# Optimization experiments

Measured on AMD Instinct MI355X. Metric: run time of the kernel, lower is better.

## Reference

```python
import jax, jax.numpy as jnp
import numpy as np

BN_EPS = 1e-5


def conv(x, w, b=None, stride=1, pad=1):
    out = jax.lax.conv_general_dilated(
        x, w, (stride, stride), [(pad, pad), (pad, pad)],
        dimension_numbers=("NCHW", "OIHW", "NCHW"))
    if b is not None:
        out = out + b[None, :, None, None]
    return out


def bn_relu(x):
    # BatchNorm2d(affine=False) in training mode: per-channel batch stats
    mean = jnp.mean(x, axis=(0, 2, 3), keepdims=True)
    var = jnp.var(x, axis=(0, 2, 3), keepdims=True)
    return jax.nn.relu((x - mean) * jax.lax.rsqrt(var + BN_EPS))


def deform_conv(x, offset, w, b, stride, pad=1):
    # torchvision DeformConv2d semantics, 3x3 kernel, dilation=1
    B, C, H, W = x.shape
    O = w.shape[0]
    K = 9
    Ho, Wo = offset.shape[2], offset.shape[3]
    off = offset.reshape(B, K, 2, Ho, Wo)  # (dy, dx) per kernel tap
    ky, kx = jnp.meshgrid(jnp.arange(3), jnp.arange(3), indexing="ij")
    ky = ky.reshape(K).astype(x.dtype)
    kx = kx.reshape(K).astype(x.dtype)
    oy = (jnp.arange(Ho) * stride - pad).astype(x.dtype)
    ox = (jnp.arange(Wo) * stride - pad).astype(x.dtype)
    # sampling coords [B,K,Ho,Wo]
    ys = oy[None, None, :, None] + ky[None, :, None, None] + off[:, :, 0]
    xs = ox[None, None, None, :] + kx[None, :, None, None] + off[:, :, 1]
    y0 = jnp.floor(ys)
    x0 = jnp.floor(xs)
    wy1 = ys - y0
    wx1 = xs - x0
    imf = x.reshape(B, C, H * W)

    def gather(iy, ix):
        valid = (iy >= 0) & (iy <= H - 1) & (ix >= 0) & (ix <= W - 1)
        iyc = jnp.clip(iy, 0, H - 1).astype(jnp.int32)
        ixc = jnp.clip(ix, 0, W - 1).astype(jnp.int32)
        lin = iyc * W + ixc  # [B,K,Ho,Wo]
        g = jax.vmap(lambda im, li: im[:, li])(imf, lin)  # [B,C,K,Ho,Wo]
        return g * valid[:, None].astype(x.dtype)

    sampled = (gather(y0, x0) * ((1 - wy1) * (1 - wx1))[:, None]
               + gather(y0, x0 + 1) * ((1 - wy1) * wx1)[:, None]
               + gather(y0 + 1, x0) * (wy1 * (1 - wx1))[:, None]
               + gather(y0 + 1, x0 + 1) * (wy1 * wx1)[:, None])
    out = jnp.einsum("ock,bckhw->bohw", w.reshape(O, C, K), sampled)
    return out + b[None, :, None, None]


def avgpool4(x):
    B, C, H, W = x.shape
    return x.reshape(B, C, H // 4, 4, W // 4, 4).mean(axis=(3, 5))


def setup_inputs() -> dict:
    key = jax.random.key(0)
    ks = jax.random.split(key, 20)
    n = jax.random.normal
    s = 0.05
    return {
        "x": n(ks[0], (8, 3, 640, 640), jnp.float32),
        "w_off1": n(ks[1], (18, 3, 3, 3), jnp.float32) * s,
        "b_off1": jnp.zeros((18,), jnp.float32),
        "w_d1": n(ks[2], (64, 3, 3, 3), jnp.float32) * s,
        "b_d1": jnp.zeros((64,), jnp.float32),
        "w_skip": n(ks[3], (64, 3, 1, 1), jnp.float32) * s,
        "b_skip": jnp.zeros((64,), jnp.float32),
        "w_bl1": n(ks[4], (64, 64, 3, 3), jnp.float32) * s,
        "w_bl2": n(ks[5], (64, 64, 3, 3), jnp.float32) * s,
        "w_off2": n(ks[6], (18, 64, 3, 3), jnp.float32) * s,
        "b_off2": jnp.zeros((18,), jnp.float32),
        "w_d2": n(ks[7], (64, 64, 3, 3), jnp.float32) * s,
        "b_d2": jnp.zeros((64,), jnp.float32),
        "w_off3": n(ks[8], (18, 64, 3, 3), jnp.float32) * s,
        "b_off3": jnp.zeros((18,), jnp.float32),
        "w_d3": n(ks[9], (256, 64, 3, 3), jnp.float32) * s,
        "b_d3": jnp.zeros((256,), jnp.float32),
    }


def reference(x, w_off1, b_off1, w_d1, b_d1, w_skip, b_skip, w_bl1, w_bl2,
              w_off2, b_off2, w_d2, b_d2, w_off3, b_off3, w_d3, b_d3):
    offset1 = conv(x, w_off1, b_off1, stride=4)
    d1 = deform_conv(x, offset1, w_d1, b_d1, stride=4)
    skip = conv(avgpool4(x), w_skip, b_skip, stride=1, pad=0)
    f = bn_relu(conv(d1 + skip, w_bl1))
    feat_1_4 = bn_relu(conv(f, w_bl2))
    offset2 = conv(feat_1_4, w_off2, b_off2, stride=2)
    feat_1_8 = deform_conv(feat_1_4, offset2, w_d2, b_d2, stride=2)
    offset3 = conv(feat_1_8, w_off3, b_off3, stride=2)
    feat_1_16 = deform_conv(feat_1_8, offset3, w_d3, b_d3, stride=2)
    return (feat_1_4, feat_1_8, feat_1_16)
```

## Files before the change

### kernel.cpp

```cpp
#include <hip/hip_runtime.h>
#include <hip/hip_bf16.h>
#include <math.h>

#define TPB 256

typedef __attribute__((ext_vector_type(8))) short bf16x8_t;
typedef __attribute__((ext_vector_type(4))) float f32x4_t;
typedef __attribute__((ext_vector_type(4))) int i32x4_t;
typedef __attribute__((ext_vector_type(4))) unsigned short u16x4_t;

static __device__ __forceinline__ float bf16_to_f(unsigned short s) {
    union { unsigned u; float f; } cv;
    cv.u = ((unsigned)s) << 16;
    return cv.f;
}
static __device__ __forceinline__ short f_to_bf16(float v) {
    __hip_bfloat16 h = __float2bfloat16(v);
    return *(short*)&h;
}

__global__ void repack_frag_kernel(const float* __restrict__ w,
                                   short* __restrict__ wtf,
                                   int Oreal, int NFRAG)
{
    int idx = blockIdx.x * TPB + threadIdx.x;
    int total = 18 * NFRAG * 64 * 8;
    if (idx >= total) return;
    int j    = idx & 7;
    int lane = (idx >> 3) & 63;
    int t    = idx >> 9;
    int ocf  = t % NFRAG;
    int kc   = t / NFRAG;
    int oc   = ocf * 16 + (lane & 15);
    int tap  = kc >> 1;
    int ic   = (kc & 1) * 32 + (lane >> 4) * 8 + j;
    float v = 0.f;
    if (oc < Oreal)
        v = w[((size_t)(oc * 64 + ic)) * 9 + tap];
    wtf[idx] = f_to_bf16(v);
}

__global__ __launch_bounds__(256, 2) void conv3x3_mfma_kernel(
    const short* __restrict__ xh,
    const short* __restrict__ wt,
    short* __restrict__ outh,
    float* __restrict__ stats,
    const float* __restrict__ zp)
{
    __shared__ short tile[2816 * 8];
    __shared__ float sstat[128];
    const int H = 160, W = 160, HW = 25600;
    int blk = blockIdx.x;
    int b  = blk / 100;
    int r  = blk % 100;
    int y0 = (r / 10) * 16;
    int x0 = (r % 10) * 16;
    const int tid = threadIdx.x;
    const short* inb = xh + (size_t)b * HW * 64;

#pragma unroll
    for (int it = 0; it < 11; ++it) {
        int item = it * 256 + tid;
        int c8  = item & 7;
        int pix = item >> 3;
        int row = pix / 18;
        int col = pix - row * 18;
        int y = y0 + row - 1;
        int x = x0 + col - 1;
        bool ok = (pix < 324) & (y >= 0) & (y < H) & (x >= 0) & (x < W);
        const short* src = ok
            ? &inb[((size_t)y * W + x) * 64 + ((c8 ^ (col & 7)) << 3)]
            : (const short*)zp;
        *(bf16x8_t*)&tile[item * 8] = *(const bf16x8_t*)src;
    }
    if (tid < 128) sstat[tid] = 0.f;
    __syncthreads();

    const int wv  = tid >> 6;
    const int l   = tid & 63;
    const int l15 = l & 15;
    const int lg  = l >> 4;

    f32x4_t acc[4][4];
#pragma unroll
    for (int i = 0; i < 4; ++i)
#pragma unroll
        for (int j = 0; j < 4; ++j)
            acc[i][j] = (f32x4_t){0.f, 0.f, 0.f, 0.f};

    bf16x8_t bfp[2][4], afp[2][4];
#pragma unroll
    for (int nf = 0; nf < 4; ++nf)
        bfp[0][nf] = *(const bf16x8_t*)(wt + (((size_t)(0 * 4 + nf)) * 64 + l) * 8);
    {
        int colr = l15;
        int chunk = lg ^ (colr & 7);
#pragma unroll
        for (int mf = 0; mf < 4; ++mf)
            afp[0][mf] = *(const bf16x8_t*)&tile[((wv * 4 + mf) * 18 + colr) * 64 + chunk * 8];
    }
#pragma unroll
    for (int kc = 0; kc < 18; ++kc) {
        const int cur = kc & 1, nxt = cur ^ 1;
        if (kc + 1 < 18) {
            int kn = kc + 1;
#pragma unroll
            for (int nf = 0; nf < 4; ++nf)
                bfp[nxt][nf] = *(const bf16x8_t*)(wt + (((size_t)(kn * 4 + nf)) * 64 + l) * 8);
            int tap = kn >> 1;
            int dy = tap / 3, dx = tap % 3;
            int colr = l15 + dx;
            int chunk = (((kn & 1) << 2) + lg) ^ (colr & 7);
#pragma unroll
            for (int mf = 0; mf < 4; ++mf)
                afp[nxt][mf] = *(const bf16x8_t*)&tile[((wv * 4 + mf + dy) * 18 + colr) * 64 + chunk * 8];
        }
#pragma unroll
        for (int mf = 0; mf < 4; ++mf)
#pragma unroll
            for (int nf = 0; nf < 4; ++nf)
                acc[mf][nf] = __builtin_amdgcn_mfma_f32_16x16x32_bf16(
                    afp[cur][mf], bfp[cur][nf], acc[mf][nf], 0, 0, 0);
    }

    __syncthreads();
#pragma unroll
    for (int mf = 0; mf < 4; ++mf) {
        int py = wv * 4 + mf;
#pragma unroll
        for (int nf = 0; nf < 4; ++nf) {
            int oc = nf * 16 + l15;
#pragma unroll
            for (int k = 0; k < 4; ++k)
                tile[((py * 16) + lg * 4 + k) * 64 + oc] = f_to_bf16(acc[mf][nf][k]);
        }
    }
    __syncthreads();
    short* outb = outh + (size_t)b * HW * 64;
#pragma unroll
    for (int j = 0; j < 8; ++j) {
        int item = j * 256 + tid;
        int c8  = item & 7;
        int pix = item >> 3;
        int py  = pix >> 4, px = pix & 15;
        *(bf16x8_t*)&outb[((size_t)(y0 + py) * W + x0 + px) * 64 + c8 * 8] =
            *(bf16x8_t*)&tile[pix * 64 + c8 * 8];
    }

#pragma unroll
    for (int nf = 0; nf < 4; ++nf) {
        float s = 0.f, s2 = 0.f;
#pragma unroll
        for (int mf = 0; mf < 4; ++mf)
#pragma unroll
            for (int k = 0; k < 4; ++k) {
                float v = acc[mf][nf][k];
                s += v; s2 += v * v;
            }
        s  += __shfl_xor(s, 16, 64);  s  += __shfl_xor(s, 32, 64);
        s2 += __shfl_xor(s2, 16, 64); s2 += __shfl_xor(s2, 32, 64);
        if (lg == 0) {
            int oc = nf * 16 + l15;
            atomicAdd(&sstat[oc], s);
            atomicAdd(&sstat[64 + oc], s2);
        }
    }
    __syncthreads();
    float* st = stats + (size_t)(blockIdx.x & 7) * 128;
    if (tid < 128) atomicAdd(&st[tid], sstat[tid]);
}

__global__ void nchw_to_nhwc_bf16_kernel(const float* __restrict__ in,
                                         short* __restrict__ out, int HW)
{
    __shared__ short tile[64][66];
    int nchunks = HW >> 6;
    int b  = blockIdx.x / nchunks;
    int p0 = (blockIdx.x % nchunks) << 6;
    int tid = threadIdx.x;
#pragma unroll
    for (int rep = 0; rep < 16; ++rep) {
        int item = rep * 256 + tid;
        int c = item >> 6, p = item & 63;
        tile[p][c] = f_to_bf16(in[((size_t)b * 64 + c) * HW + p0 + p]);
    }
    __syncthreads();
#pragma unroll
    for (int rep = 0; rep < 16; ++rep) {
        int item = rep * 256 + tid;
        int p = item >> 6, c = item & 63;
        out[((size_t)b * HW + p0 + p) * 64 + c] = tile[p][c];
    }
}

__global__ void bn_apply_elem_kernel(const short* __restrict__ in,
                                     const float* __restrict__ stats,
                                     short* __restrict__ outh,
                                     float invN)
{
    __shared__ float sm[64], sr[64];
    int tid = threadIdx.x;
    if (tid < 64) {
        float s = 0.f, s2 = 0.f;
#pragma unroll
        for (int k = 0; k < 8; ++k) {
            s  += stats[k * 128 + tid];
            s2 += stats[k * 128 + 64 + tid];
        }
        float mean = s * invN;
        float var  = s2 * invN - mean * mean;
        sm[tid] = mean;
        sr[tid] = rsqrtf(var + 1e-5f);
    }
    __syncthreads();
    int item = blockIdx.x * TPB + tid;
    int c0 = (item & 7) * 8;
    bf16x8_t v = *(const bf16x8_t*)&in[(size_t)item * 8];
    bf16x8_t o;
#pragma unroll
    for (int j = 0; j < 8; ++j) {
        float f = (bf16_to_f((unsigned short)v[j]) - sm[c0 + j]) * sr[c0 + j];
        o[j] = f_to_bf16(f > 0.f ? f : 0.f);
    }
    *(bf16x8_t*)&outh[(size_t)item * 8] = o;
}

__global__ void bn_apply_dual_kernel(const short* __restrict__ in,
                                     const float* __restrict__ stats,
                                     float* __restrict__ out,
                                     short* __restrict__ outh,
                                     int HW, float invN)
{
    __shared__ float ftile[64][65];
    __shared__ float sm[64], sr[64];
    int nchunks = HW >> 6;
    int b  = blockIdx.x / nchunks;
    int p0 = (blockIdx.x % nchunks) << 6;
    int tid = threadIdx.x;
    if (tid < 64) {
        float s = 0.f, s2 = 0.f;
#pragma unroll
        for (int k = 0; k < 8; ++k) {
            s  += stats[k * 128 + tid];
            s2 += stats[k * 128 + 64 + tid];
        }
        float mean = s * invN;
        float var  = s2 * invN - mean * mean;
        sm[tid] = mean;
        sr[tid] = rsqrtf(var + 1e-5f);
    }
    __syncthreads();
#pragma unroll
    for (int it = 0; it < 2; ++it) {
        int item = it * 256 + tid;
        int p = item >> 3, c0 = (item & 7) * 8;
        size_t gi = ((size_t)(b * HW + p0 + p)) * 64 + c0;
        bf16x8_t v = *(const bf16x8_t*)&in[gi];
        bf16x8_t o;
#pragma unroll
        for (int j = 0; j < 8; ++j) {
            float f = (bf16_to_f((unsigned short)v[j]) - sm[c0 + j]) * sr[c0 + j];
            f = f > 0.f ? f : 0.f;
            ftile[p][c0 + j] = f;
            o[j] = f_to_bf16(f);
        }
        *(bf16x8_t*)&outh[gi] = o;
    }
    __syncthreads();
#pragma unroll
    for (int rep = 0; rep < 16; ++rep) {
        int item = rep * 256 + tid;
        int c = item >> 6, p = item & 63;
        out[((size_t)b * 64 + c) * HW + p0 + p] = ftile[p][c];
    }
}

__global__ void x_to_nhwc4_kernel(const float* __restrict__ in,
                                  float* __restrict__ out)
{
    int idx = blockIdx.x * TPB + threadIdx.x;
    const int HW = 640 * 640;
    if (idx >= 8 * HW) return;
    int b = idx / HW, p = idx % HW;
    f32x4_t v;
    v[0] = in[((size_t)b * 3 + 0) * HW + p];
    v[1] = in[((size_t)b * 3 + 1) * HW + p];
    v[2] = in[((size_t)b * 3 + 2) * HW + p];
    v[3] = 0.f;
    *(f32x4_t*)&out[(size_t)idx * 4] = v;
}

__global__ void offset1_kernel(const float* __restrict__ x4,
                               const float* __restrict__ w,
                               const float* __restrict__ bias,
                               float* __restrict__ out)
{
    const int H = 640, W = 640, HW = 25600;
    int idx = blockIdx.x * TPB + threadIdx.x;
    if (idx >= 8 * HW) return;
    int b = idx / HW, r = idx % HW;
    int ho = r / 160, wo = r % 160;

    float acc[18];
#pragma unroll
    for (int o = 0; o < 18; ++o) acc[o] = bias[o];

    const float* xb = x4 + (size_t)b * H * W * 4;
#pragma unroll
    for (int tap = 0; tap < 9; ++tap) {
        int iy = ho * 4 - 1 + tap / 3;
        int ix = wo * 4 - 1 + tap % 3;
        if (iy < 0 || iy >= H || ix < 0 || ix >= W) continue;
        f32x4_t s = *(const f32x4_t*)&xb[((size_t)iy * W + ix) * 4];
#pragma unroll
        for (int c = 0; c < 3; ++c)
#pragma unroll
            for (int o = 0; o < 18; ++o)
                acc[o] += s[c] * w[(o * 3 + c) * 9 + tap];
    }
#pragma unroll
    for (int o = 0; o < 18; ++o)
        out[((size_t)(b * 18 + o)) * HW + r] = acc[o];
}

__global__ __launch_bounds__(256, 1) void offconv_mfma_kernel(
    const short* __restrict__ xh,
    const short* __restrict__ wt,
    const float* __restrict__ bias,
    float* __restrict__ out,
    int H, int W, int Ho, int Wo)
{
    const int HW = Ho * Wo;
    const int tid = threadIdx.x;
    const int wv = tid >> 6, l = tid & 63;
    const int l15 = l & 15, lg = l >> 4;
    const int pix0 = blockIdx.x * 64 + wv * 16;
    const int b = pix0 / HW;
    const int r0 = pix0 - b * HW;

    int rp = r0 + l15;
    int ho = rp / Wo, wo = rp % Wo;
    const short* xb = xh + (size_t)b * H * W * 64;

    f32x4_t acc[2];
    acc[0] = (f32x4_t){0.f, 0.f, 0.f, 0.f};
    acc[1] = (f32x4_t){0.f, 0.f, 0.f, 0.f};

#pragma unroll 2
    for (int kc = 0; kc < 18; ++kc) {
        int tap = kc >> 1;
        int iy = ho * 2 - 1 + tap / 3;
        int ix = wo * 2 - 1 + tap % 3;
        bf16x8_t af = {};
        if (iy >= 0 && iy < H && ix >= 0 && ix < W)
            af = *(const bf16x8_t*)&xb[((size_t)iy * W + ix) * 64
                                       + (kc & 1) * 32 + lg * 8];
#pragma unroll
        for (int nf = 0; nf < 2; ++nf) {
            bf16x8_t bf = *(const bf16x8_t*)(wt + (((size_t)(kc * 2 + nf)) * 64 + l) * 8);
            acc[nf] = __builtin_amdgcn_mfma_f32_16x16x32_bf16(af, bf, acc[nf], 0, 0, 0);
        }
    }

#pragma unroll
    for (int nf = 0; nf < 2; ++nf) {
        int oc = nf * 16 + l15;
        if (oc < 18) {
            float bv = bias[oc];
            f32x4_t v = acc[nf];
            v[0] += bv; v[1] += bv; v[2] += bv; v[3] += bv;
            *(f32x4_t*)&out[((size_t)(b * 18 + oc)) * HW + r0 + lg * 4] = v;
        }
    }
}

__global__ __launch_bounds__(256, 1) void deform1_kernel(
    const float* __restrict__ x4,
    const float* __restrict__ off,
    const float* __restrict__ w,
    const float* __restrict__ bias,
    const float* __restrict__ pool,
    const float* __restrict__ wsk,
    const float* __restrict__ bsk,
    short* __restrict__ outh)
{
    const int H = 640, W = 640, Ho = 160, Wo = 160, HW = 25600;
    constexpr int P = 32;
    __shared__ float samp[P][28];
    __shared__ int   sidx[P * 9][4];
    __shared__ float swt[P * 9][4];
    const int tid = threadIdx.x;
    const int pix0 = blockIdx.x * P;
    const int b = pix0 / HW;
    const int r0 = pix0 - b * HW;

    for (int item = tid; item < P * 9; item += TPB) {
        int p = item / 9, tap = item % 9;
        int r = r0 + p, ho = r / Wo, wo = r % Wo;
        float dy = off[((size_t)(b * 18 + 2 * tap) * Ho + ho) * Wo + wo];
        float dx = off[((size_t)(b * 18 + 2 * tap + 1) * Ho + ho) * Wo + wo];
        float ys = (float)(ho * 4 - 1 + tap / 3) + dy;
        float xs = (float)(wo * 4 - 1 + tap % 3) + dx;
        float y0f = floorf(ys), x0f = floorf(xs);
        float fy = ys - y0f, fx = xs - x0f;
        int y0 = (int)y0f, x0 = (int)x0f;
        float wts[4] = {(1.f - fy) * (1.f - fx), (1.f - fy) * fx,
                        fy * (1.f - fx),          fy * fx};
#pragma unroll
        for (int j = 0; j < 4; ++j) {
            int iy = y0 + (j >> 1), ix = x0 + (j & 1);
            bool v = (iy >= 0) && (iy < H) && (ix >= 0) && (ix < W);
            sidx[item][j] = v ? (iy * W + ix) : 0;
            swt[item][j]  = v ? wts[j] : 0.f;
        }
    }
    __syncthreads();

    const float* xb = x4 + (size_t)b * H * W * 4;
    for (int item = tid; item < P * 9; item += TPB) {
        int p = item / 9, tap = item % 9;
        i32x4_t id4 = *(const i32x4_t*)sidx[item];
        f32x4_t w4  = *(const f32x4_t*)swt[item];
        f32x4_t a0 = *(const f32x4_t*)&xb[(size_t)(unsigned)id4[0] * 4];
        f32x4_t a1 = *(const f32x4_t*)&xb[(size_t)(unsigned)id4[1] * 4];
        f32x4_t a2 = *(const f32x4_t*)&xb[(size_t)(unsigned)id4[2] * 4];
        f32x4_t a3 = *(const f32x4_t*)&xb[(size_t)(unsigned)id4[3] * 4];
        samp[p][0 * 9 + tap] = w4[0]*a0[0] + w4[1]*a1[0] + w4[2]*a2[0] + w4[3]*a3[0];
        samp[p][1 * 9 + tap] = w4[0]*a0[1] + w4[1]*a1[1] + w4[2]*a2[1] + w4[3]*a3[1];
        samp[p][2 * 9 + tap] = w4[0]*a0[2] + w4[1]*a1[2] + w4[2]*a2[2] + w4[3]*a3[2];
    }
    __syncthreads();

    int g = tid >> 6;
    int o = tid & 63;
    float acc[8];
#pragma unroll
    for (int pi = 0; pi < 8; ++pi) acc[pi] = bias[o] + bsk[o];
#pragma unroll
    for (int c = 0; c < 3; ++c)
#pragma unroll
        for (int k = 0; k < 9; ++k) {
            float wv = w[((size_t)(o * 3 + c)) * 9 + k];
#pragma unroll
            for (int pi = 0; pi < 8; ++pi)
                acc[pi] += wv * samp[g * 8 + pi][c * 9 + k];
        }
#pragma unroll
    for (int pi = 0; pi < 8; ++pi) {
        int r = r0 + g * 8 + pi;
        float sv = wsk[o * 3 + 0] * pool[(size_t)(b * 3 + 0) * HW + r]
                 + wsk[o * 3 + 1] * pool[(size_t)(b * 3 + 1) * HW + r]
                 + wsk[o * 3 + 2] * pool[(size_t)(b * 3 + 2) * HW + r];
        outh[((size_t)(b * HW + r)) * 64 + o] = f_to_bf16(acc[pi] + sv);
    }
}

template <int O>
__global__ __launch_bounds__(256, 1) void deform_mfma_kernel(
    const short* __restrict__ xh,
    const float* __restrict__ off,
    const short* __restrict__ wt,
    const float* __restrict__ bias,
    float* __restrict__ out,
    int H, int W, int Ho, int Wo, int stride)
{
    constexpr int NF = O / 64;
    constexpr int NFRAG = O / 16;
    constexpr int P  = 32;
    __shared__ alignas(16) short samp[P * 576];
    __shared__ int   sidx[P * 9][4];
    __shared__ float swt[P * 9][4];

    const int tid = threadIdx.x;
    const int HW = Ho * Wo;
    const int pix0 = blockIdx.x * P;
    const int b = pix0 / HW;
    const int r0 = pix0 - b * HW;

    for (int item = tid; item < P * 9; item += TPB) {
        int p = item / 9, tap = item % 9;
        int r = r0 + p, ho = r / Wo, wo = r % Wo;
        float dy = off[((size_t)(b * 18 + 2 * tap) * Ho + ho) * Wo + wo];
        float dx = off[((size_t)(b * 18 + 2 * tap + 1) * Ho + ho) * Wo + wo];
        float ys = (float)(ho * stride - 1 + tap / 3) + dy;
        float xs = (float)(wo * stride - 1 + tap % 3) + dx;
        float y0f = floorf(ys), x0f = floorf(xs);
        float fy = ys - y0f, fx = xs - x0f;
        int y0 = (int)y0f, x0 = (int)x0f;
        float wts[4] = {(1.f - fy) * (1.f - fx), (1.f - fy) * fx,
                        fy * (1.f - fx),          fy * fx};
#pragma unroll
        for (int j = 0; j < 4; ++j) {
            int iy = y0 + (j >> 1), ix = x0 + (j & 1);
            bool v = (iy >= 0) && (iy < H) && (ix >= 0) && (ix < W);
            sidx[item][j] = v ? (iy * W + ix) : 0;
            swt[item][j]  = v ? wts[j] : 0.f;
        }
    }
    __syncthreads();

    {
        const int grp = tid >> 4;
        const int ic  = (tid & 15) * 4;
        const short* xb = xh + (size_t)b * H * W * 64;
#pragma unroll 3
        for (int i = 0; i < 18; ++i) {
            int e = grp * 18 + i;
            int p = e / 9, tap = e % 9;
            i32x4_t id4 = *(const i32x4_t*)sidx[e];
            f32x4_t w4  = *(const f32x4_t*)swt[e];
            u16x4_t u0 = *(const u16x4_t*)&xb[(size_t)(unsigned)id4[0] * 64 + ic];
            u16x4_t u1 = *(const u16x4_t*)&xb[(size_t)(unsigned)id4[1] * 64 + ic];
            u16x4_t u2 = *(const u16x4_t*)&xb[(size_t)(unsigned)id4[2] * 64 + ic];
            u16x4_t u3 = *(const u16x4_t*)&xb[(size_t)(unsigned)id4[3] * 64 + ic];
            float v0 = w4[0]*bf16_to_f(u0[0]) + w4[1]*bf16_to_f(u1[0])
                     + w4[2]*bf16_to_f(u2[0]) + w4[3]*bf16_to_f(u3[0]);
            float v1 = w4[0]*bf16_to_f(u0[1]) + w4[1]*bf16_to_f(u1[1])
                     + w4[2]*bf16_to_f(u2[1]) + w4[3]*bf16_to_f(u3[1]);
            float v2 = w4[0]*bf16_to_f(u0[2]) + w4[1]*bf16_to_f(u1[2])
                     + w4[2]*bf16_to_f(u2[2]) + w4[3]*bf16_to_f(u3[2]);
            float v3 = w4[0]*bf16_to_f(u0[3]) + w4[1]*bf16_to_f(u1[3])
                     + w4[2]*bf16_to_f(u2[3]) + w4[3]*bf16_to_f(u3[3]);
            int sw = (tap * 8 + ((ic >> 3) ^ (p & 7))) * 8 + (ic & 7);
            short* dst = &samp[p * 576 + sw];
            dst[0] = f_to_bf16(v0);
            dst[1] = f_to_bf16(v1);
            dst[2] = f_to_bf16(v2);
            dst[3] = f_to_bf16(v3);
        }
    }
    __syncthreads();

    const int wv = tid >> 6;
    const int l  = tid & 63;
    const int l15 = l & 15, lg = l >> 4;
    f32x4_t acc[2][NF];
#pragma unroll
    for (int mf = 0; mf < 2; ++mf)
#pragma unroll
        for (int nf = 0; nf < NF; ++nf)
            acc[mf][nf] = (f32x4_t){0.f, 0.f, 0.f, 0.f};

#pragma unroll 2
    for (int kc = 0; kc < 18; ++kc) {
        int tap = kc >> 1;
        int low = (((kc & 1) << 2) | lg) ^ (l15 & 7);
        bf16x8_t af0 = *(const bf16x8_t*)&samp[l15 * 576 + (tap * 8 + low) * 8];
        bf16x8_t af1 = *(const bf16x8_t*)&samp[(l15 + 16) * 576 + (tap * 8 + low) * 8];
#pragma unroll
        for (int nf = 0; nf < NF; ++nf) {
            int ocf = wv * NF + nf;
            bf16x8_t bf = *(const bf16x8_t*)(wt + (((size_t)(kc * NFRAG + ocf)) * 64 + l) * 8);
            acc[0][nf] = __builtin_amdgcn_mfma_f32_16x16x32_bf16(af0, bf, acc[0][nf], 0, 0, 0);
            acc[1][nf] = __builtin_amdgcn_mfma_f32_16x16x32_bf16(af1, bf, acc[1][nf], 0, 0, 0);
        }
    }

#pragma unroll
    for (int mf = 0; mf < 2; ++mf)
#pragma unroll
        for (int nf = 0; nf < NF; ++nf) {
            int oc = (wv * NF + nf) * 16 + l15;
            float bv = bias[oc];
            f32x4_t v = acc[mf][nf];
            v[0] += bv; v[1] += bv; v[2] += bv; v[3] += bv;
            *(f32x4_t*)&out[((size_t)(b * O + oc)) * HW + r0 + mf * 16 + lg * 4] = v;
        }
}

__global__ void avgpool4_kernel(const float* __restrict__ in,
                                float* __restrict__ out,
                                int BC, int Ho, int Wo, int H, int W)
{
    int idx = blockIdx.x * TPB + threadIdx.x;
    int total = BC * Ho * Wo;
    if (idx >= total) return;
    int wo = idx % Wo;
    int t = idx / Wo;
    int ho = t % Ho;
    int bc = t / Ho;
    const float* xp = in + (size_t)bc * H * W + (ho * 4) * W + wo * 4;
    float s = 0.f;
#pragma unroll
    for (int i = 0; i < 4; ++i)
#pragma unroll
        for (int j = 0; j < 4; ++j)
            s += xp[i * W + j];
    out[idx] = s * (1.0f / 16.0f);
}

__global__ void zero_stats_kernel(float* __restrict__ stats)
{
    int i = threadIdx.x;
#pragma unroll
    for (int k = 0; k < 8; ++k) stats[k * 256 + i] = 0.f;
    stats[2048 + i] = 0.f;
    stats[2048 + 256 + i] = 0.f;
}

extern "C" void kernel_launch(void* const* d_in, const int* in_sizes, int n_in,
                              void* d_out, int out_size, void* d_ws, size_t ws_size,
                              hipStream_t stream)
{
    const float* x      = (const float*)d_in[0];
    const float* w_off1 = (const float*)d_in[1];
    const float* b_off1 = (const float*)d_in[2];
    const float* w_d1   = (const float*)d_in[3];
    const float* b_d1   = (const float*)d_in[4];
    const float* w_skip = (const float*)d_in[5];
    const float* b_skip = (const float*)d_in[6];
    const float* w_bl1  = (const float*)d_in[7];
    const float* w_bl2  = (const float*)d_in[8];
    const float* w_off2 = (const float*)d_in[9];
    const float* b_off2 = (const float*)d_in[10];
    const float* w_d2   = (const float*)d_in[11];
    const float* b_d2   = (const float*)d_in[12];
    const float* w_off3 = (const float*)d_in[13];
    const float* b_off3 = (const float*)d_in[14];
    const float* w_d3   = (const float*)d_in[15];
    const float* b_d3   = (const float*)d_in[16];

    const int B = 8;
    float* A     = (float*)d_ws;
    float* bufB  = A + 3686400;
    float* bufC  = bufB + 13107200;

    short* hB   = (short*)bufB;
    short* hC   = (short*)bufC;
    float* pool = bufB + 8000000;

    short* wt1    = (short*)(A + 1000000);
    short* wt2    = wt1 + 18 * 4 * 512;
    short* wtd2   = (short*)(A + 1500000);
    short* wtd3   = (short*)(A + 1550000);
    short* wtoff2 = (short*)(A + 1700000);
    short* wtoff3 = (short*)(A + 1712000);
    float* stats1 = A + 1800000;
    float* stats2 = stats1 + 1024;
    float* zpage  = stats1 + 2048;

    float* out0 = (float*)d_out;
    float* out1 = out0 + 13107200;
    float* out2 = out1 + 3276800;

    const float invN = 1.0f / (B * 25600);

    x_to_nhwc4_kernel<<<(8 * 409600 + TPB - 1) / TPB, TPB, 0, stream>>>(x, bufC);

    offset1_kernel<<<(8 * 25600 + TPB - 1) / TPB, TPB, 0, stream>>>(
        bufC, w_off1, b_off1, A);

    avgpool4_kernel<<<(B * 3 * 25600 + TPB - 1) / TPB, TPB, 0, stream>>>(
        x, pool, B * 3, 160, 160, 640, 640);

    deform1_kernel<<<8 * 25600 / 32, TPB, 0, stream>>>(
        bufC, A, w_d1, b_d1, pool, w_skip, b_skip, hB);

    repack_frag_kernel<<<(18 * 4 * 512 + TPB - 1) / TPB, TPB, 0, stream>>>(w_bl1, wt1, 64, 4);
    repack_frag_kernel<<<(18 * 4 * 512 + TPB - 1) / TPB, TPB, 0, stream>>>(w_bl2, wt2, 64, 4);
    repack_frag_kernel<<<(18 * 4 * 512 + TPB - 1) / TPB, TPB, 0, stream>>>(w_d2, wtd2, 64, 4);
    repack_frag_kernel<<<(18 * 16 * 512 + TPB - 1) / TPB, TPB, 0, stream>>>(w_d3, wtd3, 256, 16);
    repack_frag_kernel<<<(18 * 2 * 512 + TPB - 1) / TPB, TPB, 0, stream>>>(w_off2, wtoff2, 18, 2);
    repack_frag_kernel<<<(18 * 2 * 512 + TPB - 1) / TPB, TPB, 0, stream>>>(w_off3, wtoff3, 18, 2);
    zero_stats_kernel<<<1, 256, 0, stream>>>(stats1);

    conv3x3_mfma_kernel<<<800, TPB, 0, stream>>>(hB, wt1, hC, stats1, zpage);

    bn_apply_elem_kernel<<<8 * 25600 * 8 / TPB, TPB, 0, stream>>>(
        hC, stats1, hB, invN);

    conv3x3_mfma_kernel<<<800, TPB, 0, stream>>>(hB, wt2, hC, stats2, zpage);

    bn_apply_dual_kernel<<<8 * 400, TPB, 0, stream>>>(
        hC, stats2, out0, hB, 25600, invN);

    offconv_mfma_kernel<<<8 * 6400 / 64, TPB, 0, stream>>>(
        hB, wtoff2, b_off2, A, 160, 160, 80, 80);

    deform_mfma_kernel<64><<<8 * 6400 / 32, TPB, 0, stream>>>(
        hB, A, wtd2, b_d2, out1, 160, 160, 80, 80, 2);

    nchw_to_nhwc_bf16_kernel<<<8 * (6400 / 64), TPB, 0, stream>>>(out1, hC, 6400);

    offconv_mfma_kernel<<<8 * 1600 / 64, TPB, 0, stream>>>(
        hC, wtoff3, b_off3, A, 80, 80, 40, 40);

    deform_mfma_kernel<256><<<8 * 1600 / 32, TPB, 0, stream>>>(
        hC, A, wtd3, b_d3, out2, 80, 80, 40, 40, 2);
}
```

Baseline: 251.8 us.

## Fuse BN-ReLU into second conv prologue and offset conv into deform1

```diff
diff --git a/kernel.cpp b/kernel.cpp
--- a/kernel.cpp
+++ b/kernel.cpp
@@ -40,15 +40,19 @@
     wtf[idx] = f_to_bf16(v);
 }
 
+template <int NORM>
 __global__ __launch_bounds__(256, 2) void conv3x3_mfma_kernel(
     const short* __restrict__ xh,
     const short* __restrict__ wt,
     short* __restrict__ outh,
     float* __restrict__ stats,
+    const float* __restrict__ stats_in,
+    float invN,
     const float* __restrict__ zp)
 {
     __shared__ short tile[2816 * 8];
     __shared__ float sstat[128];
+    __shared__ float sm[64], sr[64];
     const int H = 160, W = 160, HW = 25600;
     int blk = blockIdx.x;
     int b  = blk / 100;
@@ -57,6 +61,23 @@
     int x0 = (r % 10) * 16;
     const int tid = threadIdx.x;
     const short* inb = xh + (size_t)b * HW * 64;
+
+    if (tid < 128) sstat[tid] = 0.f;
+    if (NORM) {
+        if (tid < 64) {
+            float s = 0.f, s2 = 0.f;
+#pragma unroll
+            for (int k = 0; k < 8; ++k) {
+                s  += stats_in[k * 128 + tid];
+                s2 += stats_in[k * 128 + 64 + tid];
+            }
+            float mean = s * invN;
+            float var  = s2 * invN - mean * mean;
+            sm[tid] = mean;
+            sr[tid] = rsqrtf(var + 1e-5f);
+        }
+        __syncthreads();
+    }
 
 #pragma unroll
     for (int it = 0; it < 11; ++it) {
@@ -68,12 +89,24 @@
         int y = y0 + row - 1;
         int x = x0 + col - 1;
         bool ok = (pix < 324) & (y >= 0) & (y < H) & (x >= 0) & (x < W);
+        int cs = c8 ^ (col & 7);
         const short* src = ok
-            ? &inb[((size_t)y * W + x) * 64 + ((c8 ^ (col & 7)) << 3)]
+            ? &inb[((size_t)y * W + x) * 64 + (cs << 3)]
             : (const short*)zp;
-        *(bf16x8_t*)&tile[item * 8] = *(const bf16x8_t*)src;
-    }
-    if (tid < 128) sstat[tid] = 0.f;
+        bf16x8_t v = *(const bf16x8_t*)src;
+        if (NORM) {
+            int cs8 = cs << 3;
+            bf16x8_t o;
+#pragma unroll
+            for (int j = 0; j < 8; ++j) {
+                float f = (bf16_to_f((unsigned short)v[j]) - sm[cs8 + j]) * sr[cs8 + j];
+                f = f > 0.f ? f : 0.f;
+                o[j] = ok ? f_to_bf16(f) : (short)0;
+            }
+            v = o;
+        }
+        *(bf16x8_t*)&tile[item * 8] = v;
+    }
     __syncthreads();
 
     const int wv  = tid >> 6;
@@ -193,38 +226,6 @@
     }
 }
 
-__global__ void bn_apply_elem_kernel(const short* __restrict__ in,
-                                     const float* __restrict__ stats,
-                                     short* __restrict__ outh,
-                                     float invN)
-{
-    __shared__ float sm[64], sr[64];
-    int tid = threadIdx.x;
-    if (tid < 64) {
-        float s = 0.f, s2 = 0.f;
-#pragma unroll
-        for (int k = 0; k < 8; ++k) {
-            s  += stats[k * 128 + tid];
-            s2 += stats[k * 128 + 64 + tid];
-        }
-        float mean = s * invN;
-        float var  = s2 * invN - mean * mean;
-        sm[tid] = mean;
-        sr[tid] = rsqrtf(var + 1e-5f);
-    }
-    __syncthreads();
-    int item = blockIdx.x * TPB + tid;
-    int c0 = (item & 7) * 8;
-    bf16x8_t v = *(const bf16x8_t*)&in[(size_t)item * 8];
-    bf16x8_t o;
-#pragma unroll
-    for (int j = 0; j < 8; ++j) {
-        float f = (bf16_to_f((unsigned short)v[j]) - sm[c0 + j]) * sr[c0 + j];
-        o[j] = f_to_bf16(f > 0.f ? f : 0.f);
-    }
-    *(bf16x8_t*)&outh[(size_t)item * 8] = o;
-}
-
 __global__ void bn_apply_dual_kernel(const short* __restrict__ in,
                                      const float* __restrict__ stats,
                                      float* __restrict__ out,
@@ -290,39 +291,6 @@
     *(f32x4_t*)&out[(size_t)idx * 4] = v;
 }
 
-__global__ void offset1_kernel(const float* __restrict__ x4,
-                               const float* __restrict__ w,
-                               const float* __restrict__ bias,
-                               float* __restrict__ out)
-{
-    const int H = 640, W = 640, HW = 25600;
-    int idx = blockIdx.x * TPB + threadIdx.x;
-    if (idx >= 8 * HW) return;
-    int b = idx / HW, r = idx % HW;
-    int ho = r / 160, wo = r % 160;
-
-    float acc[18];
-#pragma unroll
-    for (int o = 0; o < 18; ++o) acc[o] = bias[o];
-
-    const float* xb = x4 + (size_t)b * H * W * 4;
-#pragma unroll
-    for (int tap = 0; tap < 9; ++tap) {
-        int iy = ho * 4 - 1 + tap / 3;
-        int ix = wo * 4 - 1 + tap % 3;
-        if (iy < 0 || iy >= H || ix < 0 || ix >= W) continue;
-        f32x4_t s = *(const f32x4_t*)&xb[((size_t)iy * W + ix) * 4];
-#pragma unroll
-        for (int c = 0; c < 3; ++c)
-#pragma unroll
-            for (int o = 0; o < 18; ++o)
-                acc[o] += s[c] * w[(o * 3 + c) * 9 + tap];
-    }
-#pragma unroll
-    for (int o = 0; o < 18; ++o)
-        out[((size_t)(b * 18 + o)) * HW + r] = acc[o];
-}
-
 __global__ __launch_bounds__(256, 1) void offconv_mfma_kernel(
     const short* __restrict__ xh,
     const short* __restrict__ wt,
@@ -376,7 +344,8 @@
 
 __global__ __launch_bounds__(256, 1) void deform1_kernel(
     const float* __restrict__ x4,
-    const float* __restrict__ off,
+    const float* __restrict__ wof,
+    const float* __restrict__ bof,
     const float* __restrict__ w,
     const float* __restrict__ bias,
     const float* __restrict__ pool,
@@ -386,6 +355,10 @@
 {
     const int H = 640, W = 640, Ho = 160, Wo = 160, HW = 25600;
     constexpr int P = 32;
+    __shared__ float xtap[P * 9][4];
+    __shared__ float swof[486];
+    __shared__ float sbof[18];
+    __shared__ float off1[P][18];
     __shared__ float samp[P][28];
     __shared__ int   sidx[P * 9][4];
     __shared__ float swt[P * 9][4];
@@ -393,12 +366,41 @@
     const int pix0 = blockIdx.x * P;
     const int b = pix0 / HW;
     const int r0 = pix0 - b * HW;
+    const float* xb = x4 + (size_t)b * H * W * 4;
 
     for (int item = tid; item < P * 9; item += TPB) {
         int p = item / 9, tap = item % 9;
         int r = r0 + p, ho = r / Wo, wo = r % Wo;
-        float dy = off[((size_t)(b * 18 + 2 * tap) * Ho + ho) * Wo + wo];
-        float dx = off[((size_t)(b * 18 + 2 * tap + 1) * Ho + ho) * Wo + wo];
+        int iy = ho * 4 - 1 + tap / 3;
+        int ix = wo * 4 - 1 + tap % 3;
+        f32x4_t s = (f32x4_t){0.f, 0.f, 0.f, 0.f};
+        if (iy >= 0 && iy < H && ix >= 0 && ix < W)
+            s = *(const f32x4_t*)&xb[((size_t)iy * W + ix) * 4];
+        *(f32x4_t*)xtap[item] = s;
+    }
+    for (int item = tid; item < 486; item += TPB) swof[item] = wof[item];
+    if (tid < 18) sbof[tid] = bof[tid];
+    __syncthreads();
+
+    for (int item = tid; item < P * 18; item += TPB) {
+        int p = item / 18, o = item % 18;
+        float acc = sbof[o];
+#pragma unroll
+        for (int tap = 0; tap < 9; ++tap) {
+            const float* xt = xtap[p * 9 + tap];
+#pragma unroll
+            for (int c = 0; c < 3; ++c)
+                acc += xt[c] * swof[(o * 3 + c) * 9 + tap];
+        }
+        off1[p][o] = acc;
+    }
+    __syncthreads();
+
+    for (int item = tid; item < P * 9; item += TPB) {
+        int p = item / 9, tap = item % 9;
+        int r = r0 + p, ho = r / Wo, wo = r % Wo;
+        float dy = off1[p][2 * tap];
+        float dx = off1[p][2 * tap + 1];
         float ys = (float)(ho * 4 - 1 + tap / 3) + dy;
         float xs = (float)(wo * 4 - 1 + tap % 3) + dx;
         float y0f = floorf(ys), x0f = floorf(xs);
@@ -416,7 +418,6 @@
     }
     __syncthreads();
 
-    const float* xb = x4 + (size_t)b * H * W * 4;
     for (int item = tid; item < P * 9; item += TPB) {
         int p = item / 9, tap = item % 9;
         i32x4_t id4 = *(const i32x4_t*)sidx[item];
@@ -647,14 +648,8 @@
 
     x_to_nhwc4_kernel<<<(8 * 409600 + TPB - 1) / TPB, TPB, 0, stream>>>(x, bufC);
 
-    offset1_kernel<<<(8 * 25600 + TPB - 1) / TPB, TPB, 0, stream>>>(
-        bufC, w_off1, b_off1, A);
-
     avgpool4_kernel<<<(B * 3 * 25600 + TPB - 1) / TPB, TPB, 0, stream>>>(
         x, pool, B * 3, 160, 160, 640, 640);
-
-    deform1_kernel<<<8 * 25600 / 32, TPB, 0, stream>>>(
-        bufC, A, w_d1, b_d1, pool, w_skip, b_skip, hB);
 
     repack_frag_kernel<<<(18 * 4 * 512 + TPB - 1) / TPB, TPB, 0, stream>>>(w_bl1, wt1, 64, 4);
     repack_frag_kernel<<<(18 * 4 * 512 + TPB - 1) / TPB, TPB, 0, stream>>>(w_bl2, wt2, 64, 4);
@@ -664,27 +659,29 @@
     repack_frag_kernel<<<(18 * 2 * 512 + TPB - 1) / TPB, TPB, 0, stream>>>(w_off3, wtoff3, 18, 2);
     zero_stats_kernel<<<1, 256, 0, stream>>>(stats1);
 
-    conv3x3_mfma_kernel<<<800, TPB, 0, stream>>>(hB, wt1, hC, stats1, zpage);
-
-    bn_apply_elem_kernel<<<8 * 25600 * 8 / TPB, TPB, 0, stream>>>(
-        hC, stats1, hB, invN);
-
-    conv3x3_mfma_kernel<<<800, TPB, 0, stream>>>(hB, wt2, hC, stats2, zpage);
+    deform1_kernel<<<8 * 25600 / 32, TPB, 0, stream>>>(
+        bufC, w_off1, b_off1, w_d1, b_d1, pool, w_skip, b_skip, hB);
+
+    conv3x3_mfma_kernel<0><<<800, TPB, 0, stream>>>(
+        hB, wt1, hC, stats1, nullptr, invN, zpage);
+
+    conv3x3_mfma_kernel<1><<<800, TPB, 0, stream>>>(
+        hC, wt2, hB, stats2, stats1, invN, zpage);
 
     bn_apply_dual_kernel<<<8 * 400, TPB, 0, stream>>>(
-        hC, stats2, out0, hB, 25600, invN);
+        hB, stats2, out0, hC, 25600, invN);
 
     offconv_mfma_kernel<<<8 * 6400 / 64, TPB, 0, stream>>>(
-        hB, wtoff2, b_off2, A, 160, 160, 80, 80);
+        hC, wtoff2, b_off2, A, 160, 160, 80, 80);
 
     deform_mfma_kernel<64><<<8 * 6400 / 32, TPB, 0, stream>>>(
-        hB, A, wtd2, b_d2, out1, 160, 160, 80, 80, 2);
-
-    nchw_to_nhwc_bf16_kernel<<<8 * (6400 / 64), TPB, 0, stream>>>(out1, hC, 6400);
+        hC, A, wtd2, b_d2, out1, 160, 160, 80, 80, 2);
+
+    nchw_to_nhwc_bf16_kernel<<<8 * (6400 / 64), TPB, 0, stream>>>(out1, hB, 6400);
 
     offconv_mfma_kernel<<<8 * 1600 / 64, TPB, 0, stream>>>(
-        hC, wtoff3, b_off3, A, 80, 80, 40, 40);
+        hB, wtoff3, b_off3, A, 80, 80, 40, 40);
 
     deform_mfma_kernel<256><<<8 * 1600 / 32, TPB, 0, stream>>>(
-        hC, A, wtd3, b_d3, out2, 80, 80, 40, 40, 2);
-}
+        hB, A, wtd3, b_d3, out2, 80, 80, 40, 40, 2);
+}
```

New measurement: 245.4 us. 2.6% less time.
